# Kernel optimization log

Hardware: AMD Instinct MI355X
Metric: run time of the kernel (lower is better)

The kernel has to match this reference:

```python
import jax, jax.numpy as jnp
import numpy as np

EPS = 1e-5


def _conv(x, w, pad):
    return jax.lax.conv_general_dilated(
        x, w, (1, 1), [(pad, pad), (pad, pad)],
        dimension_numbers=('NCHW', 'OIHW', 'NCHW'))


def _reflect_pad1(x):
    return jnp.pad(x, ((0, 0), (0, 0), (1, 1), (1, 1)), mode='reflect')


def _instance_norm(x):
    m = x.mean((2, 3), keepdims=True)
    v = x.var((2, 3), keepdims=True)  # biased, as torch InstanceNorm2d
    return (x - m) * jax.lax.rsqrt(v + EPS)


def _batch_norm(x, g, b):
    m = x.mean((0, 2, 3), keepdims=True)
    v = x.var((0, 2, 3), keepdims=True)
    return (x - m) * jax.lax.rsqrt(v + EPS) * g.reshape(1, -1, 1, 1) + b.reshape(1, -1, 1, 1)


def _dct_ortho(x):
    # DCT-II with 'ortho' norm along last axis (same math as torch_dct.dct)
    N = x.shape[-1]
    v = jnp.concatenate([x[..., ::2], x[..., 1::2][..., ::-1]], axis=-1)
    Vc = jnp.fft.fft(v)
    k = jnp.arange(N) * (np.pi / (2.0 * N))
    V = Vc.real * jnp.cos(k) + Vc.imag * jnp.sin(k)
    scale = jnp.full((N,), 1.0 / np.sqrt(N / 2.0), dtype=x.dtype).at[0].set(1.0 / np.sqrt(float(N)))
    return V * scale


def _idct_ortho(X):
    # DCT-III (inverse of ortho DCT-II) along last axis (same math as torch_dct.idct)
    N = X.shape[-1]
    scale = jnp.full((N,), np.sqrt(N / 2.0), dtype=X.dtype).at[0].set(np.sqrt(float(N)))
    Xv = X * scale
    k = jnp.arange(N) * (np.pi / (2.0 * N))
    Wr, Wi = jnp.cos(k), jnp.sin(k)
    Vti = jnp.concatenate([jnp.zeros_like(Xv[..., :1]), -Xv[..., ::-1][..., :-1]], axis=-1)
    V = (Xv * Wr - Vti * Wi) + 1j * (Xv * Wi + Vti * Wr)
    v = jnp.fft.ifft(V).real
    out = jnp.zeros_like(v)
    out = out.at[..., ::2].set(v[..., : (N + 1) // 2])
    out = out.at[..., 1::2].set(v[..., ::-1][..., : N // 2])
    return out


def setup_inputs() -> dict:
    key = jax.random.key(0)
    ks = iter(jax.random.split(key, 32))
    B, C, H, W = 4, 128, 128, 128
    R = C // 16  # SFOM ratio
    d = {'x': jax.random.normal(next(ks), (B, C, H, W), jnp.float32)}
    d['conv1_w'] = jax.random.normal(next(ks), (C, C, 3, 3), jnp.float32) * 0.05
    d['conv1_b'] = jnp.zeros((C,), jnp.float32)
    d['conv2_w'] = jax.random.normal(next(ks), (C, C, 3, 3), jnp.float32) * 0.05
    d['conv2_b'] = jnp.zeros((C,), jnp.float32)
    # SFOM spectral attention MLP (torch Linear weights: [out, in])
    d['sa_w1'] = jax.random.normal(next(ks), (R, C), jnp.float32) * 0.1
    d['sa_w2'] = jax.random.normal(next(ks), (C, R), jnp.float32) * 0.1
    # SPEM dynamic-conv pyramid: 128->32->64->128->128->64->32, k=7
    chans = [(C, 32), (32, 64), (64, 128), (128, 128), (128, 64), (64, 32)]
    for i, (ci, co) in enumerate(chans, 1):
        d[f'dw{i}'] = jax.random.normal(next(ks), (co, ci, 7, 7), jnp.float32) * (0.05 / np.sqrt(ci))
        d[f'bg{i}'] = jnp.ones((co,), jnp.float32)
        d[f'bb{i}'] = jnp.zeros((co,), jnp.float32)
    d['spem_cw'] = jax.random.normal(next(ks), (1, 32, 1, 1), jnp.float32) * 0.1
    d['spem_cb'] = jnp.zeros((1,), jnp.float32)
    return d


def reference(x, conv1_w, conv1_b, conv2_w, conv2_b, sa_w1, sa_w2,
              dw1, bg1, bb1, dw2, bg2, bb2, dw3, bg3, bb3,
              dw4, bg4, bb4, dw5, bg5, bb5, dw6, bg6, bb6,
              spem_cw, spem_cb):
    # conv1: reflect pad 1 + conv(padding=1) -> spatial grows by 2
    out = _conv(_reflect_pad1(x), conv1_w, 1) + conv1_b.reshape(1, -1, 1, 1)
    out = jax.nn.relu(_instance_norm(out))
    out = _conv(_reflect_pad1(out), conv2_w, 1) + conv2_b.reshape(1, -1, 1, 1)
    out = _instance_norm(out)
    # SFOM channel attention via DCT gating
    B, C, H, W = out.shape
    dctx = _dct_ortho(out.reshape(B, C, H * W)).reshape(B, C, H, W)
    m = dctx.mean((2, 3))  # [B, C]
    gate = jax.nn.sigmoid(jax.nn.relu(m @ sa_w1.T) @ sa_w2.T)  # [B, C]
    idctx = _idct_ortho((dctx * gate[:, :, None, None]).reshape(B, C, H * W)).reshape(B, C, H, W)
    out = jax.nn.sigmoid((out + idctx) * 0.5) * out
    # SPEM spatial attention; DynamicConv2d repeats one shared filter per sample,
    # which is mathematically identical to a plain conv with that filter.
    h = out
    for w_, g_, b_ in ((dw1, bg1, bb1), (dw2, bg2, bb2), (dw3, bg3, bb3),
                       (dw4, bg4, bb4), (dw5, bg5, bb5), (dw6, bg6, bb6)):
        h = jax.nn.relu(_batch_norm(_conv(h, w_, 3), g_, b_))
    sa = jax.nn.sigmoid(_conv(h, spem_cw, 0) + spem_cb.reshape(1, -1, 1, 1))
    return sa * out
```

## Files before the change

kernel.cpp:

```cpp
#include <hip/hip_runtime.h>
#include <math.h>

#define B_    4
#define HW1   (130*130)
#define HW2   (132*132)
#define NBUF  ((size_t)B_*128*HW2)
#define EPS_  1e-5f
#define PI_   3.14159265358979f

typedef _Float16 half8 __attribute__((ext_vector_type(8)));
typedef _Float16 half4_ __attribute__((ext_vector_type(4)));
typedef float    float4_ __attribute__((ext_vector_type(4)));

struct WPackArgs {
  const float* src[8];
  _Float16*    dst[8];
  int cout[8], cin[8], kk[8];
  int off[9];
};
__global__ void wpack_all(WPackArgs p) {
  int idx = blockIdx.x * blockDim.x + threadIdx.x;
  if (idx >= p.off[8]) return;
  int s = 0;
  while (idx >= p.off[s + 1]) ++s;
  int i = idx - p.off[s];
  int Cin = p.cin[s], K = p.kk[s];
  int KK = K * K, COG = p.cout[s] / 16;
  int j    = i & 7;
  int lane = (i >> 3) & 63;
  int rest = i >> 9;
  int g    = rest % COG; rest /= COG;
  int tap  = rest % KK;
  int cc   = rest / KK;
  int n = lane & 15, q = lane >> 4;
  int co = g * 16 + n;
  int ci = cc * 32 + q * 8 + j;
  p.dst[s][i] = (_Float16)p.src[s][((size_t)co * Cin + ci) * KK + tap];
}

__global__ void to_nhwc(const float* __restrict__ in, _Float16* __restrict__ out,
                        int C, int HW) {
  __shared__ float t[32][65];
  int b = blockIdx.z, c0 = blockIdx.y * 32, p0 = blockIdx.x * 64;
  int tid = threadIdx.x;
  for (int i = 0; i < 8; ++i) {
    int e = i * 256 + tid; int cl = e >> 6, pl = e & 63;
    int p = p0 + pl;
    float v = 0.f;
    if (p < HW) v = in[((size_t)b * C + c0 + cl) * HW + p];
    t[cl][pl] = v;
  }
  __syncthreads();
  for (int i = 0; i < 8; ++i) {
    int e = i * 256 + tid; int pl = e >> 5, cl = e & 31;
    int p = p0 + pl;
    if (p < HW) out[((size_t)b * HW + p) * C + c0 + cl] = (_Float16)t[cl][pl];
  }
}

__global__ void zerok(float* p, int n) {
  int i = blockIdx.x * blockDim.x + threadIdx.x;
  if (i < n) p[i] = 0.f;
}

template<int CIN, int COUT, int K, int HIN, int HOUT, bool REFLECT, int AFF, bool RELU, bool POB>
__global__ __launch_bounds__(256, 2) void conv_mfma(
    const _Float16* __restrict__ act, const _Float16* __restrict__ wp,
    const float* __restrict__ sums_in, const float* __restrict__ gam,
    const float* __restrict__ bet, float invn, float* __restrict__ sums_out,
    _Float16* __restrict__ out) {
  constexpr int NWC = (COUT >= 64) ? 2 : 1;
  constexpr int WCO = COUT / NWC;
  constexpr int MR  = WCO / 16;
  constexpr int NWR = 4 / NWC;
  constexpr int ROWS = NWR * 4;
  constexpr int PADc = (K - 1) / 2;
  constexpr int IR = ROWS + K - 1;
  constexpr int XW = 16 + K - 1;
  constexpr int CH = IR * 4 * XW;
  constexpr int COG = COUT / 16;
  constexpr int KK = K * K;
  constexpr int XT = (HOUT + 15) / 16;

  __shared__ half8 smem[CH];
  __shared__ float2 snorm[CIN];
  __shared__ float bsum[COUT * 2];

  const int xt = blockIdx.x % XT, yt = blockIdx.x / XT;
  const int x0 = xt * 16, y0 = yt * ROWS;
  const int b = blockIdx.z;
  const int tid = threadIdx.x;
  const int lane = tid & 63, w = tid >> 6;
  const int wc = (NWC == 2) ? (w & 1) : 0;
  const int wr = (NWC == 2) ? (w >> 1) : w;
  const int n = lane & 15, q = lane >> 4;

  if (AFF) {
    if (tid < CIN) {
      int idx = (AFF == 1 ? b * CIN : 0) + tid;
      float m  = sums_in[idx * 2] * invn;
      float vr = sums_in[idx * 2 + 1] * invn - m * m;
      float sc = rsqrtf(vr + EPS_);
      if (AFF == 2) sc *= gam[tid];
      float sh = (AFF == 2 ? bet[tid] : 0.f) - m * sc;
      snorm[tid] = make_float2(sc, sh);
    }
  }
  if (tid < COUT) { bsum[tid * 2] = 0.f; bsum[tid * 2 + 1] = 0.f; }

  float4_ acc[MR][4];
#pragma unroll
  for (int mi = 0; mi < MR; ++mi)
#pragma unroll
    for (int ni = 0; ni < 4; ++ni)
#pragma unroll
      for (int j = 0; j < 4; ++j) acc[mi][ni][j] = 0.f;

  const _Float16* actb = act + (size_t)b * HIN * HIN * CIN;

  for (int cc = 0; cc < CIN / 32; ++cc) {
    __syncthreads();
    float nsc[8], nsh[8];
    if (AFF) {
      int cb2 = cc * 32 + (tid & 3) * 8;
#pragma unroll
      for (int j = 0; j < 8; ++j) { float2 t = snorm[cb2 + j]; nsc[j] = t.x; nsh[j] = t.y; }
    }
    for (int e = tid; e < CH; e += 256) {
      int qq = e & 3, rx = e >> 2;
      int row = rx / XW, lx = rx % XW;
      int ty = y0 + row - PADc;
      int tx = x0 + lx - PADc;
      bool ok; int iy, ix;
      if (REFLECT) {
        ok = (ty >= 0 && ty < HIN + 2 && tx >= 0 && tx < HIN + 2);
        iy = (ty == 0) ? 1 : (ty == HIN + 1 ? HIN - 2 : ty - 1);
        ix = (tx == 0) ? 1 : (tx == HIN + 1 ? HIN - 2 : tx - 1);
      } else {
        ok = (ty >= 0 && ty < HIN && tx >= 0 && tx < HIN);
        iy = ty; ix = tx;
      }
      half8 v;
#pragma unroll
      for (int j = 0; j < 8; ++j) v[j] = (_Float16)0.f;
      if (ok) {
        v = *(const half8*)(actb + ((size_t)iy * HIN + ix) * CIN + cc * 32 + qq * 8);
        if (AFF) {
#pragma unroll
          for (int j = 0; j < 8; ++j) {
            float f = (float)v[j] * nsc[j] + nsh[j];
            if (RELU) f = fmaxf(f, 0.f);
            v[j] = (_Float16)f;
          }
        }
      }
      smem[(row * 4 + qq) * XW + lx] = v;
    }
    __syncthreads();
    auto ldA = [&](int tap, half8* a) {
#pragma unroll
      for (int mi = 0; mi < MR; ++mi) {
        int g = wc * MR + mi;
        a[mi] = *(const half8*)(wp + (((size_t)(cc * KK + tap) * COG + g) * 64 + lane) * 8);
      }
    };
    auto ldB = [&](int tap, half8* c) {
      int ky = tap / K, kx = tap % K;
#pragma unroll
      for (int ni = 0; ni < 4; ++ni)
        c[ni] = smem[((wr * 4 + ni + ky) * 4 + q) * XW + n + kx];
    };
    auto domf = [&](half8* a, half8* c) {
#pragma unroll
      for (int mi = 0; mi < MR; ++mi)
#pragma unroll
        for (int ni = 0; ni < 4; ++ni)
          acc[mi][ni] = __builtin_amdgcn_mfma_f32_16x16x32_f16(a[mi], c[ni], acc[mi][ni], 0, 0, 0);
    };
    half8 a0[MR], a1[MR], c0[4], c1[4];
    ldA(0, a0); ldB(0, c0);
    for (int tap = 0; tap + 1 < KK; tap += 2) {
      ldA(tap + 1, a1); ldB(tap + 1, c1);
      domf(a0, c0);
      ldA(tap + 2, a0); ldB(tap + 2, c0);
      domf(a1, c1);
    }
    domf(a0, c0);
  }

  const bool xv = (x0 + n) < HOUT;
#pragma unroll
  for (int mi = 0; mi < MR; ++mi) {
#pragma unroll
    for (int j = 0; j < 4; ++j) {
      float s = 0.f, s2 = 0.f;
#pragma unroll
      for (int ni = 0; ni < 4; ++ni) {
        int y = y0 + wr * 4 + ni;
        float f = acc[mi][ni][j];
        bool v = xv && (y < HOUT);
        s  += v ? f : 0.f;
        s2 += v ? f * f : 0.f;
      }
#pragma unroll
      for (int off = 1; off < 16; off <<= 1) {
        s  += __shfl_xor(s,  off, 64);
        s2 += __shfl_xor(s2, off, 64);
      }
      if (n == 0) {
        int co = wc * WCO + mi * 16 + q * 4 + j;
        atomicAdd(&bsum[co * 2],     s);
        atomicAdd(&bsum[co * 2 + 1], s2);
      }
    }
  }
  _Float16* outb = out + (size_t)b * HOUT * HOUT * COUT;
#pragma unroll
  for (int mi = 0; mi < MR; ++mi) {
#pragma unroll
    for (int ni = 0; ni < 4; ++ni) {
      int y = y0 + wr * 4 + ni, x = x0 + n;
      if (y < HOUT && x < HOUT) {
        int co = wc * WCO + mi * 16 + q * 4;
        half4_ h;
#pragma unroll
        for (int j = 0; j < 4; ++j) h[j] = (_Float16)acc[mi][ni][j];
        *(half4_*)(outb + ((size_t)y * HOUT + x) * COUT + co) = h;
      }
    }
  }
  __syncthreads();
  if (tid < COUT) {
    int idx = (POB ? b * COUT : 0) + tid;
    atomicAdd(&sums_out[idx * 2],     bsum[tid * 2]);
    atomicAdd(&sums_out[idx * 2 + 1], bsum[tid * 2 + 1]);
  }
}

__global__ void wdctk(float* __restrict__ wd, int N) {
  int i = blockIdx.x * blockDim.x + threadIdx.x;
  if (i >= N) return;
  float Nf = (float)N;
  float c2 = 0.5f * sqrtf(2.f / Nf);
  float a  = sqrtf(1.f / Nf) - c2;
  float phi = PI_ / (4.f * Nf) * (2.f * i + 1.f);
  float cot = cosf(phi) / sinf(phi);
  wd[i] = a + ((i & 1) ? -c2 : c2) * cot;
}

__global__ void mdctk(const _Float16* __restrict__ x, const float* __restrict__ wd,
                      const float* __restrict__ sums2, float invn,
                      float* __restrict__ md, int HW) {
  int b = blockIdx.z, tid = threadIdx.x;
  int c = tid & 127, pr = tid >> 7;
  int slab = blockIdx.x, nsl = gridDim.x;
  float m  = sums2[(b * 128 + c) * 2] * invn;
  float sc = rsqrtf(sums2[(b * 128 + c) * 2 + 1] * invn - m * m + EPS_);
  float sh = -m * sc;
  const _Float16* xb = x + (size_t)b * HW * 128;
  float s = 0.f;
  for (int p = slab * 2 + pr; p < HW; p += nsl * 2)
    s += ((float)xb[(size_t)p * 128 + c] * sc + sh) * wd[p];
  __shared__ float l1[256];
  l1[tid] = s;
  __syncthreads();
  if (tid < 128) atomicAdd(&md[b * 128 + c], l1[tid] + l1[tid + 128]);
}

__global__ void gatek(const float* __restrict__ md, const float* __restrict__ w1,
                      const float* __restrict__ w2, float* __restrict__ gate) {
  __shared__ float t1[4][8];
  int tid = threadIdx.x;
  const float invN = 1.f / (float)HW2;
  if (tid < 32) {
    int b = tid >> 3, r = tid & 7;
    float s = 0.f;
    for (int c = 0; c < 128; ++c) s += md[b * 128 + c] * invN * w1[r * 128 + c];
    t1[b][r] = fmaxf(s, 0.f);
  }
  __syncthreads();
  int b = tid >> 7, c = tid & 127;
  float s = 0.f;
#pragma unroll
  for (int r = 0; r < 8; ++r) s += t1[b][r] * w2[c * 8 + r];
  gate[tid] = 1.f / (1.f + expf(-s));
}

__global__ void sfomk(const _Float16* __restrict__ x, const float* __restrict__ sums2,
                      float invn, const float* __restrict__ gate,
                      _Float16* __restrict__ o, int HW) {
  size_t idx = (size_t)blockIdx.x * blockDim.x + threadIdx.x;
  size_t tot = (size_t)4 * HW * 16;
  if (idx >= tot) return;
  int cg = (int)(idx % 16);
  size_t bp = idx / 16;
  int b = (int)(bp / HW);
  half8 v = *(const half8*)(x + bp * 128 + cg * 8);
  half8 r;
#pragma unroll
  for (int j = 0; j < 8; ++j) {
    int c = cg * 8 + j;
    float m  = sums2[(b * 128 + c) * 2] * invn;
    float sc = rsqrtf(sums2[(b * 128 + c) * 2 + 1] * invn - m * m + EPS_);
    float f = (float)v[j] * sc - m * sc;
    float g = gate[b * 128 + c];
    float s = 1.f / (1.f + expf(-(f * (1.f + g) * 0.5f)));
    r[j] = (_Float16)(s * f);
  }
  *(half8*)(o + bp * 128 + cg * 8) = r;
}

__global__ void sak(const _Float16* __restrict__ h, const float* __restrict__ sums6,
                    float invn, const float* __restrict__ gam, const float* __restrict__ bet,
                    const float* __restrict__ cw, const float* __restrict__ cb,
                    float* __restrict__ sa) {
  __shared__ float ssc[32], ssh[32];
  int tid = threadIdx.x;
  if (tid < 32) {
    float m  = sums6[tid * 2] * invn;
    float sc = rsqrtf(sums6[tid * 2 + 1] * invn - m * m + EPS_) * gam[tid];
    ssc[tid] = sc;
    ssh[tid] = bet[tid] - m * sc;
  }
  __syncthreads();
  int idx = blockIdx.x * blockDim.x + tid;
  if (idx >= 4 * HW2) return;
  const _Float16* p = h + (size_t)idx * 32;
  float s = cb[0];
#pragma unroll
  for (int c = 0; c < 32; ++c)
    s += fmaxf((float)p[c] * ssc[c] + ssh[c], 0.f) * cw[c];
  sa[idx] = 1.f / (1.f + expf(-s));
}

__global__ void finalt(const _Float16* __restrict__ o, const float* __restrict__ sa,
                       float* __restrict__ out) {
  __shared__ float t[32][65];
  int b = blockIdx.z, c0 = blockIdx.y * 32, p0 = blockIdx.x * 64;
  int tid = threadIdx.x;
  for (int i = 0; i < 8; ++i) {
    int e = i * 256 + tid; int pl = e >> 5, cl = e & 31;
    int p = p0 + pl;
    if (p < HW2)
      t[cl][pl] = (float)o[((size_t)b * HW2 + p) * 128 + c0 + cl] * sa[b * HW2 + p];
  }
  __syncthreads();
  for (int i = 0; i < 8; ++i) {
    int e = i * 256 + tid; int cl = e >> 6, pl = e & 63;
    int p = p0 + pl;
    if (p < HW2)
      out[((size_t)b * 128 + c0 + cl) * HW2 + p] = t[cl][pl];
  }
}

extern "C" void kernel_launch(void* const* d_in, const int* in_sizes, int n_in,
                              void* d_out, int out_size, void* d_ws, size_t ws_size,
                              hipStream_t stream) {
  const float* x     = (const float*)d_in[0];
  const float* c1w   = (const float*)d_in[1];
  const float* c2w   = (const float*)d_in[3];
  const float* sa_w1 = (const float*)d_in[5];
  const float* sa_w2 = (const float*)d_in[6];
  const float* dw[6] = {(const float*)d_in[7],  (const float*)d_in[10], (const float*)d_in[13],
                        (const float*)d_in[16], (const float*)d_in[19], (const float*)d_in[22]};
  const float* bg[6] = {(const float*)d_in[8],  (const float*)d_in[11], (const float*)d_in[14],
                        (const float*)d_in[17], (const float*)d_in[20], (const float*)d_in[23]};
  const float* bb[6] = {(const float*)d_in[9],  (const float*)d_in[12], (const float*)d_in[15],
                        (const float*)d_in[18], (const float*)d_in[21], (const float*)d_in[24]};
  const float* cw    = (const float*)d_in[25];
  const float* cb    = (const float*)d_in[26];
  float* out = (float*)d_out;

  char* wsp = (char*)d_ws;
  auto alloc = [&](size_t bytes) { char* p = wsp; wsp += (bytes + 255) & ~(size_t)255; return p; };
  _Float16* B0 = (_Float16*)alloc(NBUF * 2);
  _Float16* B1 = (_Float16*)alloc(NBUF * 2);
  _Float16* B2 = (_Float16*)alloc(NBUF * 2);
  _Float16* B3 = (_Float16*)alloc(NBUF * 2);
  _Float16* wp_c1 = (_Float16*)alloc((size_t)128 * 128 * 9 * 2);
  _Float16* wp_c2 = (_Float16*)alloc((size_t)128 * 128 * 9 * 2);
  const int sci[6] = {128, 32, 64, 128, 128, 64};
  const int sco[6] = {32, 64, 128, 128, 64, 32};
  _Float16* wp_d[6];
  for (int i = 0; i < 6; ++i) wp_d[i] = (_Float16*)alloc((size_t)sco[i] * sci[i] * 49 * 2);
  float* SUMS = (float*)alloc(8704 * 4);
  float* s_c1 = SUMS;
  float* s_c2 = SUMS + 1024;
  float* s_l[6];
  for (int i = 0; i < 6; ++i) s_l[i] = SUMS + 2048 + i * 1024;
  float* md   = SUMS + 8192;
  float* gate = (float*)alloc(512 * 4);
  float* wd   = (float*)alloc((size_t)HW2 * 4);
  float* sa   = (float*)alloc((size_t)4 * HW2 * 4);

  {
    WPackArgs p;
    p.src[0] = c1w; p.dst[0] = wp_c1; p.cout[0] = 128; p.cin[0] = 128; p.kk[0] = 3;
    p.src[1] = c2w; p.dst[1] = wp_c2; p.cout[1] = 128; p.cin[1] = 128; p.kk[1] = 3;
    for (int i = 0; i < 6; ++i) {
      p.src[2 + i] = dw[i]; p.dst[2 + i] = wp_d[i];
      p.cout[2 + i] = sco[i]; p.cin[2 + i] = sci[i]; p.kk[2 + i] = 7;
    }
    p.off[0] = 0;
    for (int i = 0; i < 8; ++i) p.off[i + 1] = p.off[i] + p.cout[i] * p.cin[i] * p.kk[i] * p.kk[i];
    wpack_all<<<(p.off[8] + 255) / 256, 256, 0, stream>>>(p);
  }

  to_nhwc<<<dim3(16384 / 64, 4, 4), 256, 0, stream>>>(x, B0, 128, 16384);
  zerok<<<34, 256, 0, stream>>>(SUMS, 8704);

  const float i1 = 1.f / (float)HW1, i2 = 1.f / (float)HW2, ib = 1.f / (4.f * HW2);

  conv_mfma<128, 128, 3, 128, 130, true, 0, false, true><<<dim3(9 * 17, 1, 4), 256, 0, stream>>>(
      B0, wp_c1, nullptr, nullptr, nullptr, 0.f, s_c1, B1);
  conv_mfma<128, 128, 3, 130, 132, true, 1, true, true><<<dim3(9 * 17, 1, 4), 256, 0, stream>>>(
      B1, wp_c2, s_c1, nullptr, nullptr, i1, s_c2, B2);

  wdctk<<<(HW2 + 255) / 256, 256, 0, stream>>>(wd, HW2);
  mdctk<<<dim3(128, 1, 4), 256, 0, stream>>>(B2, wd, s_c2, i2, md, HW2);
  gatek<<<1, 512, 0, stream>>>(md, sa_w1, sa_w2, gate);
  { size_t tot = (size_t)4 * HW2 * 16;
    sfomk<<<(int)((tot + 255) / 256), 256, 0, stream>>>(B2, s_c2, i2, gate, B3, HW2); }

  conv_mfma<128, 32, 7, 132, 132, false, 0, false, false><<<dim3(9 * 9, 1, 4), 256, 0, stream>>>(
      B3, wp_d[0], nullptr, nullptr, nullptr, 0.f, s_l[0], B0);
  conv_mfma<32, 64, 7, 132, 132, false, 2, true, false><<<dim3(9 * 17, 1, 4), 256, 0, stream>>>(
      B0, wp_d[1], s_l[0], bg[0], bb[0], ib, s_l[1], B1);
  conv_mfma<64, 128, 7, 132, 132, false, 2, true, false><<<dim3(9 * 17, 1, 4), 256, 0, stream>>>(
      B1, wp_d[2], s_l[1], bg[1], bb[1], ib, s_l[2], B0);
  conv_mfma<128, 128, 7, 132, 132, false, 2, true, false><<<dim3(9 * 17, 1, 4), 256, 0, stream>>>(
      B0, wp_d[3], s_l[2], bg[2], bb[2], ib, s_l[3], B1);
  conv_mfma<128, 64, 7, 132, 132, false, 2, true, false><<<dim3(9 * 17, 1, 4), 256, 0, stream>>>(
      B1, wp_d[4], s_l[3], bg[3], bb[3], ib, s_l[4], B0);
  conv_mfma<64, 32, 7, 132, 132, false, 2, true, false><<<dim3(9 * 9, 1, 4), 256, 0, stream>>>(
      B0, wp_d[5], s_l[4], bg[4], bb[4], ib, s_l[5], B1);

  sak<<<(4 * HW2 + 255) / 256, 256, 0, stream>>>(B1, s_l[5], ib, bg[5], bb[5], cw, cb, sa);
  finalt<<<dim3((HW2 + 63) / 64, 4, 4), 256, 0, stream>>>(B3, sa, out);
}
```

Measured before the change: 733.7 us.

## Double-buffer conv input tiles in LDS with register prefetch and B-row reuse

The MFMA conv now loads the next channel chunk's input tile from global memory into registers before computing the current chunk, then writes it into a second LDS buffer, so global latency overlaps with MFMA work. The LDS row stride is padded to 24, and each wave handles one 8-channel quarter, with loading organised per lane. The tap loop is reordered by kx so that the K+3 B rows loaded from LDS are reused across all ky taps, which cuts LDS reads. The cost is more registers and twice the LDS per block, which could reduce occupancy at the launch bounds of 2 blocks per CU.

```diff
diff --git a/kernel.cpp b/kernel.cpp
--- a/kernel.cpp
+++ b/kernel.cpp
@@ -75,14 +75,20 @@
   constexpr int NWR = 4 / NWC;
   constexpr int ROWS = NWR * 4;
   constexpr int PADc = (K - 1) / 2;
-  constexpr int IR = ROWS + K - 1;
-  constexpr int XW = 16 + K - 1;
-  constexpr int CH = IR * 4 * XW;
+  constexpr int IR  = ROWS + K - 1;
+  constexpr int XWn = 16 + K - 1;
+  constexpr int XWs = 24;
+  constexpr int CH  = IR * 4 * XWs;
+  constexpr int NBUFS = (2 * CH * 16 <= 59000) ? 2 : 1;
+  constexpr int PERQ = IR * XWn;
+  constexpr int SMAX = (PERQ + 63) / 64;
+  constexpr int NREG = K + 3;
   constexpr int COG = COUT / 16;
   constexpr int KK = K * K;
   constexpr int XT = (HOUT + 15) / 16;
-
-  __shared__ half8 smem[CH];
+  constexpr int NC = CIN / 32;
+
+  __shared__ half8 smem[NBUFS][CH];
   __shared__ float2 snorm[CIN];
   __shared__ float bsum[COUT * 2];
 
@@ -107,6 +113,7 @@
     }
   }
   if (tid < COUT) { bsum[tid * 2] = 0.f; bsum[tid * 2 + 1] = 0.f; }
+  __syncthreads();
 
   float4_ acc[MR][4];
 #pragma unroll
@@ -118,74 +125,118 @@
 
   const _Float16* actb = act + (size_t)b * HIN * HIN * CIN;
 
-  for (int cc = 0; cc < CIN / 32; ++cc) {
-    __syncthreads();
+  auto coords = [&](int s, bool& ok, int& iy, int& ix) {
+    int row = s / XWn, lx = s % XWn;
+    int ty = y0 + row - PADc;
+    int tx = x0 + lx - PADc;
+    if (REFLECT) {
+      ok = (ty >= 0 && ty < HIN + 2 && tx >= 0 && tx < HIN + 2);
+      iy = (ty == 0) ? 1 : (ty == HIN + 1 ? HIN - 2 : ty - 1);
+      ix = (tx == 0) ? 1 : (tx == HIN + 1 ? HIN - 2 : tx - 1);
+    } else {
+      ok = (ty >= 0 && ty < HIN && tx >= 0 && tx < HIN);
+      iy = ty; ix = tx;
+    }
+  };
+  auto stage_load = [&](int cc, half8* v) {
+#pragma unroll
+    for (int i = 0; i < SMAX; ++i) {
+      int s = i * 64 + lane;
+      half8 t;
+#pragma unroll
+      for (int j = 0; j < 8; ++j) t[j] = (_Float16)0.f;
+      if (s < PERQ) {
+        bool ok; int iy, ix;
+        coords(s, ok, iy, ix);
+        if (ok) t = *(const half8*)(actb + ((size_t)iy * HIN + ix) * CIN + cc * 32 + w * 8);
+      }
+      v[i] = t;
+    }
+  };
+  auto stage_write = [&](int buf, int cc, half8* v) {
     float nsc[8], nsh[8];
     if (AFF) {
-      int cb2 = cc * 32 + (tid & 3) * 8;
-#pragma unroll
-      for (int j = 0; j < 8; ++j) { float2 t = snorm[cb2 + j]; nsc[j] = t.x; nsh[j] = t.y; }
-    }
-    for (int e = tid; e < CH; e += 256) {
-      int qq = e & 3, rx = e >> 2;
-      int row = rx / XW, lx = rx % XW;
-      int ty = y0 + row - PADc;
-      int tx = x0 + lx - PADc;
-      bool ok; int iy, ix;
-      if (REFLECT) {
-        ok = (ty >= 0 && ty < HIN + 2 && tx >= 0 && tx < HIN + 2);
-        iy = (ty == 0) ? 1 : (ty == HIN + 1 ? HIN - 2 : ty - 1);
-        ix = (tx == 0) ? 1 : (tx == HIN + 1 ? HIN - 2 : tx - 1);
-      } else {
-        ok = (ty >= 0 && ty < HIN && tx >= 0 && tx < HIN);
-        iy = ty; ix = tx;
-      }
-      half8 v;
-#pragma unroll
-      for (int j = 0; j < 8; ++j) v[j] = (_Float16)0.f;
-      if (ok) {
-        v = *(const half8*)(actb + ((size_t)iy * HIN + ix) * CIN + cc * 32 + qq * 8);
-        if (AFF) {
+#pragma unroll
+      for (int j = 0; j < 8; ++j) {
+        float2 t = snorm[cc * 32 + w * 8 + j];
+        nsc[j] = t.x; nsh[j] = t.y;
+      }
+    }
+#pragma unroll
+    for (int i = 0; i < SMAX; ++i) {
+      int s = i * 64 + lane;
+      if (s >= PERQ) break;
+      int row = s / XWn, lx = s % XWn;
+      half8 t = v[i];
+      if (AFF) {
+        bool ok; int iy, ix;
+        coords(s, ok, iy, ix);
+        if (ok) {
 #pragma unroll
           for (int j = 0; j < 8; ++j) {
-            float f = (float)v[j] * nsc[j] + nsh[j];
+            float f = (float)t[j] * nsc[j] + nsh[j];
             if (RELU) f = fmaxf(f, 0.f);
-            v[j] = (_Float16)f;
+            t[j] = (_Float16)f;
           }
         }
       }
-      smem[(row * 4 + qq) * XW + lx] = v;
-    }
-    __syncthreads();
-    auto ldA = [&](int tap, half8* a) {
+      smem[buf][(row * 4 + w) * XWs + lx] = t;
+    }
+  };
+  auto compute = [&](int buf, int cc) {
+    const int R0 = wr * 4;
+    half8 areg[2][MR];
+    auto ldA = [&](int t, half8* a) {
+      int kx = t / K, ky = t % K;
+      int tap = ky * K + kx;
 #pragma unroll
       for (int mi = 0; mi < MR; ++mi) {
         int g = wc * MR + mi;
         a[mi] = *(const half8*)(wp + (((size_t)(cc * KK + tap) * COG + g) * 64 + lane) * 8);
       }
     };
-    auto ldB = [&](int tap, half8* c) {
-      int ky = tap / K, kx = tap % K;
-#pragma unroll
-      for (int ni = 0; ni < 4; ++ni)
-        c[ni] = smem[((wr * 4 + ni + ky) * 4 + q) * XW + n + kx];
-    };
-    auto domf = [&](half8* a, half8* c) {
-#pragma unroll
-      for (int mi = 0; mi < MR; ++mi)
-#pragma unroll
-        for (int ni = 0; ni < 4; ++ni)
-          acc[mi][ni] = __builtin_amdgcn_mfma_f32_16x16x32_f16(a[mi], c[ni], acc[mi][ni], 0, 0, 0);
-    };
-    half8 a0[MR], a1[MR], c0[4], c1[4];
-    ldA(0, a0); ldB(0, c0);
-    for (int tap = 0; tap + 1 < KK; tap += 2) {
-      ldA(tap + 1, a1); ldB(tap + 1, c1);
-      domf(a0, c0);
-      ldA(tap + 2, a0); ldB(tap + 2, c0);
-      domf(a1, c1);
-    }
-    domf(a0, c0);
+    ldA(0, areg[0]);
+    if (KK > 1) ldA(1, areg[1]);
+    half8 breg[NREG];
+#pragma unroll
+    for (int kx = 0; kx < K; ++kx) {
+#pragma unroll
+      for (int ri = 0; ri < NREG; ++ri)
+        breg[ri] = smem[buf][((R0 + ri) * 4 + q) * XWs + n + kx];
+#pragma unroll
+      for (int ky = 0; ky < K; ++ky) {
+        const int t = kx * K + ky;
+#pragma unroll
+        for (int mi = 0; mi < MR; ++mi)
+#pragma unroll
+          for (int ni = 0; ni < 4; ++ni)
+            acc[mi][ni] = __builtin_amdgcn_mfma_f32_16x16x32_f16(
+                areg[t & 1][mi], breg[ky + ni], acc[mi][ni], 0, 0, 0);
+        if (t + 2 < KK) ldA(t + 2, areg[t & 1]);
+      }
+    }
+  };
+
+  half8 sv[SMAX];
+  stage_load(0, sv);
+  stage_write(0, 0, sv);
+  __syncthreads();
+#pragma unroll 1
+  for (int cc = 0; cc < NC; ++cc) {
+    bool more = (cc + 1 < NC);
+    if (NBUFS == 2) {
+      if (more) stage_load(cc + 1, sv);
+      compute(cc & 1, cc);
+      if (more) { stage_write((cc + 1) & 1, cc + 1, sv); __syncthreads(); }
+    } else {
+      compute(0, cc);
+      if (more) {
+        stage_load(cc + 1, sv);
+        __syncthreads();
+        stage_write(0, cc + 1, sv);
+        __syncthreads();
+      }
+    }
   }
 
   const bool xv = (x0 + n) < HOUT;
```

Result: slower. 1.210 ms (+64.9%).

## Use 2-wave blocks with 8 rows per wave to reuse weight fragments

Applied to the files above, without the earlier changes.

For convs with COUT>=64, the block drops from 4 waves to 2, and each wave now computes 8 output rows instead of 4 while keeping the same block tile. Each weight (A) fragment loaded from global memory now feeds twice as many MFMAs. The tap loop is rescheduled to interleave the two row halves with prefetched A and B loads. The trade-off is double the accumulator registers per wave and fewer waves per block to hide latency, so occupancy and latency hiding may suffer.

```diff
diff --git a/kernel.cpp b/kernel.cpp
--- a/kernel.cpp
+++ b/kernel.cpp
@@ -64,23 +64,27 @@
 }
 
 template<int CIN, int COUT, int K, int HIN, int HOUT, bool REFLECT, int AFF, bool RELU, bool POB>
-__global__ __launch_bounds__(256, 2) void conv_mfma(
+__global__ __launch_bounds__((COUT >= 64) ? 128 : 256, 2) void conv_mfma(
     const _Float16* __restrict__ act, const _Float16* __restrict__ wp,
     const float* __restrict__ sums_in, const float* __restrict__ gam,
     const float* __restrict__ bet, float invn, float* __restrict__ sums_out,
     _Float16* __restrict__ out) {
+  constexpr int NT  = (COUT >= 64) ? 128 : 256;
+  constexpr int NWAV = NT / 64;
   constexpr int NWC = (COUT >= 64) ? 2 : 1;
   constexpr int WCO = COUT / NWC;
   constexpr int MR  = WCO / 16;
-  constexpr int NWR = 4 / NWC;
-  constexpr int ROWS = NWR * 4;
+  constexpr int NWR = NWAV / NWC;
+  constexpr int NR  = (COUT >= 64) ? 8 : 4;
+  constexpr int NH  = NR / 4;
+  constexpr int ROWS = NWR * NR;
   constexpr int PADc = (K - 1) / 2;
-  constexpr int IR = ROWS + K - 1;
-  constexpr int XW = 16 + K - 1;
-  constexpr int CH = IR * 4 * XW;
+  constexpr int IR  = ROWS + K - 1;
+  constexpr int XW  = 16 + K - 1;
+  constexpr int CH  = IR * 4 * XW;
   constexpr int COG = COUT / 16;
-  constexpr int KK = K * K;
-  constexpr int XT = (HOUT + 15) / 16;
+  constexpr int KK  = K * K;
+  constexpr int XT  = (HOUT + 15) / 16;
 
   __shared__ half8 smem[CH];
   __shared__ float2 snorm[CIN];
@@ -91,8 +95,8 @@
   const int b = blockIdx.z;
   const int tid = threadIdx.x;
   const int lane = tid & 63, w = tid >> 6;
-  const int wc = (NWC == 2) ? (w & 1) : 0;
-  const int wr = (NWC == 2) ? (w >> 1) : w;
+  const int wc = (NWC == 2) ? w : 0;
+  const int wr = (NWC == 2) ? 0 : w;
   const int n = lane & 15, q = lane >> 4;
 
   if (AFF) {
@@ -108,11 +112,11 @@
   }
   if (tid < COUT) { bsum[tid * 2] = 0.f; bsum[tid * 2 + 1] = 0.f; }
 
-  float4_ acc[MR][4];
+  float4_ acc[MR][NR];
 #pragma unroll
   for (int mi = 0; mi < MR; ++mi)
 #pragma unroll
-    for (int ni = 0; ni < 4; ++ni)
+    for (int ni = 0; ni < NR; ++ni)
 #pragma unroll
       for (int j = 0; j < 4; ++j) acc[mi][ni][j] = 0.f;
 
@@ -126,7 +130,7 @@
 #pragma unroll
       for (int j = 0; j < 8; ++j) { float2 t = snorm[cb2 + j]; nsc[j] = t.x; nsh[j] = t.y; }
     }
-    for (int e = tid; e < CH; e += 256) {
+    for (int e = tid; e < CH; e += NT) {
       int qq = e & 3, rx = e >> 2;
       int row = rx / XW, lx = rx % XW;
       int ty = y0 + row - PADc;
@@ -157,35 +161,62 @@
       smem[(row * 4 + qq) * XW + lx] = v;
     }
     __syncthreads();
-    auto ldA = [&](int tap, half8* a) {
-#pragma unroll
-      for (int mi = 0; mi < MR; ++mi) {
-        int g = wc * MR + mi;
-        a[mi] = *(const half8*)(wp + (((size_t)(cc * KK + tap) * COG + g) * 64 + lane) * 8);
-      }
-    };
-    auto ldB = [&](int tap, half8* c) {
-      int ky = tap / K, kx = tap % K;
-#pragma unroll
-      for (int ni = 0; ni < 4; ++ni)
-        c[ni] = smem[((wr * 4 + ni + ky) * 4 + q) * XW + n + kx];
-    };
-    auto domf = [&](half8* a, half8* c) {
-#pragma unroll
-      for (int mi = 0; mi < MR; ++mi)
+    {
+      auto ldA = [&](int tap, half8* a) {
+#pragma unroll
+        for (int mi = 0; mi < MR; ++mi) {
+          int g = wc * MR + mi;
+          a[mi] = *(const half8*)(wp + (((size_t)(cc * KK + tap) * COG + g) * 64 + lane) * 8);
+        }
+      };
+      auto ldBh = [&](int tap, int h, half8* c) {
+        int ky = tap / K, kx = tap % K;
+        int rbase = wr * NR + h * 4 + ky;
 #pragma unroll
         for (int ni = 0; ni < 4; ++ni)
-          acc[mi][ni] = __builtin_amdgcn_mfma_f32_16x16x32_f16(a[mi], c[ni], acc[mi][ni], 0, 0, 0);
-    };
-    half8 a0[MR], a1[MR], c0[4], c1[4];
-    ldA(0, a0); ldB(0, c0);
-    for (int tap = 0; tap + 1 < KK; tap += 2) {
-      ldA(tap + 1, a1); ldB(tap + 1, c1);
-      domf(a0, c0);
-      ldA(tap + 2, a0); ldB(tap + 2, c0);
-      domf(a1, c1);
-    }
-    domf(a0, c0);
+          c[ni] = smem[((rbase + ni) * 4 + q) * XW + n + kx];
+      };
+      auto domfh = [&](half8* a, half8* c, int h) {
+#pragma unroll
+        for (int mi = 0; mi < MR; ++mi)
+#pragma unroll
+          for (int ni = 0; ni < 4; ++ni)
+            acc[mi][h * 4 + ni] = __builtin_amdgcn_mfma_f32_16x16x32_f16(
+                a[mi], c[ni], acc[mi][h * 4 + ni], 0, 0, 0);
+      };
+      half8 a0[MR], a1[MR], c0[4], c1[4];
+      ldA(0, a0);
+      ldA(1, a1);
+      ldBh(0, 0, c0);
+      for (int tap = 0; tap + 1 < KK; tap += 2) {
+        if constexpr (NH == 2) {
+          ldBh(tap, 1, c1);
+          domfh(a0, c0, 0);
+          ldBh(tap + 1, 0, c0);
+          domfh(a0, c1, 1);
+          ldA(tap + 2, a0);
+          ldBh(tap + 1, 1, c1);
+          domfh(a1, c0, 0);
+          ldBh(tap + 2, 0, c0);
+          domfh(a1, c1, 1);
+          if (tap + 3 < KK) ldA(tap + 3, a1);
+        } else {
+          ldBh(tap + 1, 0, c1);
+          domfh(a0, c0, 0);
+          ldA(tap + 2, a0);
+          ldBh(tap + 2, 0, c0);
+          domfh(a1, c1, 0);
+          if (tap + 3 < KK) ldA(tap + 3, a1);
+        }
+      }
+      if constexpr (NH == 2) {
+        ldBh(KK - 1, 1, c1);
+        domfh(a0, c0, 0);
+        domfh(a0, c1, 1);
+      } else {
+        domfh(a0, c0, 0);
+      }
+    }
   }
 
   const bool xv = (x0 + n) < HOUT;
@@ -195,8 +226,8 @@
     for (int j = 0; j < 4; ++j) {
       float s = 0.f, s2 = 0.f;
 #pragma unroll
-      for (int ni = 0; ni < 4; ++ni) {
-        int y = y0 + wr * 4 + ni;
+      for (int ni = 0; ni < NR; ++ni) {
+        int y = y0 + wr * NR + ni;
         float f = acc[mi][ni][j];
         bool v = xv && (y < HOUT);
         s  += v ? f : 0.f;
@@ -218,8 +249,8 @@
 #pragma unroll
   for (int mi = 0; mi < MR; ++mi) {
 #pragma unroll
-    for (int ni = 0; ni < 4; ++ni) {
-      int y = y0 + wr * 4 + ni, x = x0 + n;
+    for (int ni = 0; ni < NR; ++ni) {
+      int y = y0 + wr * NR + ni, x = x0 + n;
       if (y < HOUT && x < HOUT) {
         int co = wc * WCO + mi * 16 + q * 4;
         half4_ h;
@@ -411,9 +442,9 @@
 
   const float i1 = 1.f / (float)HW1, i2 = 1.f / (float)HW2, ib = 1.f / (4.f * HW2);
 
-  conv_mfma<128, 128, 3, 128, 130, true, 0, false, true><<<dim3(9 * 17, 1, 4), 256, 0, stream>>>(
+  conv_mfma<128, 128, 3, 128, 130, true, 0, false, true><<<dim3(9 * 17, 1, 4), 128, 0, stream>>>(
       B0, wp_c1, nullptr, nullptr, nullptr, 0.f, s_c1, B1);
-  conv_mfma<128, 128, 3, 130, 132, true, 1, true, true><<<dim3(9 * 17, 1, 4), 256, 0, stream>>>(
+  conv_mfma<128, 128, 3, 130, 132, true, 1, true, true><<<dim3(9 * 17, 1, 4), 128, 0, stream>>>(
       B1, wp_c2, s_c1, nullptr, nullptr, i1, s_c2, B2);
 
   wdctk<<<(HW2 + 255) / 256, 256, 0, stream>>>(wd, HW2);
@@ -424,13 +455,13 @@
 
   conv_mfma<128, 32, 7, 132, 132, false, 0, false, false><<<dim3(9 * 9, 1, 4), 256, 0, stream>>>(
       B3, wp_d[0], nullptr, nullptr, nullptr, 0.f, s_l[0], B0);
-  conv_mfma<32, 64, 7, 132, 132, false, 2, true, false><<<dim3(9 * 17, 1, 4), 256, 0, stream>>>(
+  conv_mfma<32, 64, 7, 132, 132, false, 2, true, false><<<dim3(9 * 17, 1, 4), 128, 0, stream>>>(
       B0, wp_d[1], s_l[0], bg[0], bb[0], ib, s_l[1], B1);
-  conv_mfma<64, 128, 7, 132, 132, false, 2, true, false><<<dim3(9 * 17, 1, 4), 256, 0, stream>>>(
+  conv_mfma<64, 128, 7, 132, 132, false, 2, true, false><<<dim3(9 * 17, 1, 4), 128, 0, stream>>>(
       B1, wp_d[2], s_l[1], bg[1], bb[1], ib, s_l[2], B0);
-  conv_mfma<128, 128, 7, 132, 132, false, 2, true, false><<<dim3(9 * 17, 1, 4), 256, 0, stream>>>(
+  conv_mfma<128, 128, 7, 132, 132, false, 2, true, false><<<dim3(9 * 17, 1, 4), 128, 0, stream>>>(
       B0, wp_d[3], s_l[2], bg[2], bb[2], ib, s_l[3], B1);
-  conv_mfma<128, 64, 7, 132, 132, false, 2, true, false><<<dim3(9 * 17, 1, 4), 256, 0, stream>>>(
+  conv_mfma<128, 64, 7, 132, 132, false, 2, true, false><<<dim3(9 * 17, 1, 4), 128, 0, stream>>>(
       B1, wp_d[4], s_l[3], bg[3], bb[3], ib, s_l[4], B0);
   conv_mfma<64, 32, 7, 132, 132, false, 2, true, false><<<dim3(9 * 9, 1, 4), 256, 0, stream>>>(
       B0, wp_d[5], s_l[4], bg[4], bb[4], ib, s_l[5], B1);
```

Measured after the change: 902.9 us. 1.23x slower.
